# Performance work log

Measured on AMD Instinct MI355X. Metric: run time of the kernel, lower is better.

Reference implementation:

```python
import jax, jax.numpy as jnp
import numpy as np

NUM_NODES = 8192
IN_FEATURES = 1024
OUT_FEATURES = 512
NUM_EDGES = 262144  # avg degree 32


def setup_inputs() -> dict:
    key = jax.random.key(0)
    k_x, k_w, k_b, k_src, k_dst = jax.random.split(key, 5)
    x = jax.random.normal(k_x, (NUM_NODES, IN_FEATURES), dtype=jnp.float32)
    # torch nn.Linear layout: weight [out, in], bias [out]
    W = jax.random.normal(k_w, (OUT_FEATURES, IN_FEATURES), dtype=jnp.float32) * (1.0 / np.sqrt(IN_FEATURES))
    b = jax.random.normal(k_b, (OUT_FEATURES,), dtype=jnp.float32) * 0.01
    src = jax.random.randint(k_src, (NUM_EDGES,), 0, NUM_NODES, dtype=jnp.int64)
    dst = jax.random.randint(k_dst, (NUM_EDGES,), 0, NUM_NODES, dtype=jnp.int64)
    edge_index = jnp.stack([src, dst], axis=0)
    return {"x": x, "W": W, "b": b, "edge_index": edge_index, "num_nodes": NUM_NODES}


def reference(x, W, b, edge_index, num_nodes):
    # Faithful to the torch module: build dense adjacency from edge list
    # (duplicate edges collapse to 1.0 via assignment semantics),
    # linear, (dropout p=0 -> identity), dense adj @ hidden, relu.
    adj = jnp.zeros((num_nodes, num_nodes), dtype=x.dtype)
    adj = adj.at[edge_index[0], edge_index[1]].set(1.0)
    hidden = x @ W.T + b            # [N, out]
    support = adj @ hidden          # [N, out] aggregation over neighbors
    return jax.nn.relu(support)
```

## Files before the change

kernel.cpp:

```cpp
#include <hip/hip_runtime.h>

#define N_NODES 8192
#define IN_F    1024
#define OUT_F   512
#define N_EDGES 262144
#define STRIDE  96
#define NBLK    32

#define HID_OFF     0u
#define WB_OFF      8388608u
#define DEG_OFF     9437184u
#define COL_OFF     9469952u
#define BH_OFF      12615680u
#define BO_OFF      13664256u
#define MAX_DEG     STRIDE

typedef short  bf16x8 __attribute__((ext_vector_type(8)));
typedef float  f32x4  __attribute__((ext_vector_type(4)));

__device__ __forceinline__ unsigned f2bf(float f) {
    unsigned u = __float_as_uint(f);
    u += 0x7fffu + ((u >> 16) & 1u);
    return u >> 16;
}

__device__ __forceinline__ float bflo(unsigned u) { return __uint_as_float(u << 16); }
__device__ __forceinline__ float bfhi(unsigned u) { return __uint_as_float(u & 0xffff0000u); }

__device__ __forceinline__ void ld_lds16(const void* g, void* l) {
    __builtin_amdgcn_global_load_lds(
        (const __attribute__((address_space(1))) void*)g,
        (__attribute__((address_space(3))) void*)l, 16, 0, 0);
}

#define NW8 (OUT_F * IN_F / 8)
__global__ __launch_bounds__(256) void prep(const float* __restrict__ w,
                                            unsigned short* __restrict__ wb) {
    int i = blockIdx.x * blockDim.x + threadIdx.x;
    const f32x4* p = (const f32x4*)w + (size_t)i * 2;
    f32x4 v0 = __builtin_nontemporal_load(p);
    f32x4 v1 = __builtin_nontemporal_load(p + 1);
    uint4 o;
    o.x = f2bf(v0.x) | (f2bf(v0.y) << 16);
    o.y = f2bf(v0.z) | (f2bf(v0.w) << 16);
    o.z = f2bf(v1.x) | (f2bf(v1.y) << 16);
    o.w = f2bf(v1.z) | (f2bf(v1.w) << 16);
    *((uint4*)wb + i) = o;
}

__global__ __launch_bounds__(256) void hist_a(const int* __restrict__ src,
                                              int* __restrict__ blkhist) {
    __shared__ int h[N_NODES];
    const int b   = blockIdx.x;
    const int tid = threadIdx.x;
    for (int i = tid; i < N_NODES; i += 256) h[i] = 0;
    __syncthreads();
    const int e0 = b * (N_EDGES / NBLK);
#pragma unroll
    for (int j = 0; j < N_EDGES / NBLK / 256; ++j)
        atomicAdd(&h[src[e0 + j * 256 + tid]], 1);
    __syncthreads();
    for (int i = tid; i < N_NODES; i += 256)
        blkhist[b * N_NODES + i] = h[i];
}

__global__ __launch_bounds__(256) void scan_b(const int* __restrict__ blkhist,
                                              int* __restrict__ boff,
                                              int* __restrict__ deg) {
    const int i = blockIdx.x * 256 + threadIdx.x;
    int s = 0;
#pragma unroll
    for (int b = 0; b < NBLK; ++b) {
        int t = blkhist[b * N_NODES + i];
        boff[b * N_NODES + i] = s;
        s += t;
    }
    deg[i] = s;
}

__global__ __launch_bounds__(256) void place_c(const int* __restrict__ src,
                                               const int* __restrict__ dst,
                                               const int* __restrict__ boff,
                                               int* __restrict__ col) {
    __shared__ int h[N_NODES];
    const int b   = blockIdx.x;
    const int tid = threadIdx.x;
    for (int i = tid; i < N_NODES; i += 256) h[i] = 0;
    __syncthreads();
    const int e0 = b * (N_EDGES / NBLK);
#pragma unroll
    for (int j = 0; j < N_EDGES / NBLK / 256; ++j) {
        int e = e0 + j * 256 + tid;
        int s = src[e];
        int r = boff[b * N_NODES + s] + atomicAdd(&h[s], 1);
        if (r < STRIDE) col[s * STRIDE + r] = dst[e];
    }
}

__global__ __launch_bounds__(256, 6) void gemm_mfma(const float* __restrict__ X,
                                                    const unsigned short* __restrict__ Wb,
                                                    const float* __restrict__ bias,
                                                    unsigned short* __restrict__ H) {
    __shared__ unsigned short As[64 * 64];
    __shared__ unsigned short Bs[64 * 64];

    const int bid  = blockIdx.x;
    const int tid  = threadIdx.x;
    const int lane = tid & 63;
    const int wave = tid >> 6;
    const int row0 = (bid & 127) * 64;
    const int col0 = (bid >> 7) * 64;
    const int wm   = (wave & 1) * 32;
    const int wn   = (wave >> 1) * 32;
    const int fm   = lane & 15;
    const int fm7  = fm & 7;
    const int q    = lane >> 4;

    f32x4 acc[2][2];
#pragma unroll
    for (int i = 0; i < 2; ++i)
#pragma unroll
        for (int j = 0; j < 2; ++j) acc[i][j] = (f32x4)0.f;

    const int ar   = tid >> 2;
    const int ak4  = tid & 3;
    const int ar7  = ar & 7;
    unsigned short* As_w0 = As + ar * 64 + ((ak4 * 2)     ^ ar7) * 8;
    unsigned short* As_w1 = As + ar * 64 + ((ak4 * 2 + 1) ^ ar7) * 8;
    const float* xrow = &X[(size_t)(row0 + ar) * IN_F + ak4 * 16];

    const int br = tid >> 3;
    const int bk = ((tid & 7) ^ (br & 7)) * 8;

    for (int k0 = 0; k0 < IN_F; k0 += 64) {
        const f32x4* px = (const f32x4*)(xrow + k0);
        f32x4 v0 = px[0], v1 = px[1], v2 = px[2], v3 = px[3];
        ld_lds16(Wb + (size_t)(col0 + br) * IN_F + k0 + bk,      Bs + tid * 8);
        ld_lds16(Wb + (size_t)(col0 + br + 32) * IN_F + k0 + bk, Bs + (tid + 256) * 8);
        uint4 pa, pb;
        pa.x = f2bf(v0.x) | (f2bf(v0.y) << 16);
        pa.y = f2bf(v0.z) | (f2bf(v0.w) << 16);
        pa.z = f2bf(v1.x) | (f2bf(v1.y) << 16);
        pa.w = f2bf(v1.z) | (f2bf(v1.w) << 16);
        pb.x = f2bf(v2.x) | (f2bf(v2.y) << 16);
        pb.y = f2bf(v2.z) | (f2bf(v2.w) << 16);
        pb.z = f2bf(v3.x) | (f2bf(v3.y) << 16);
        pb.w = f2bf(v3.z) | (f2bf(v3.w) << 16);
        *(uint4*)As_w0 = pa;
        *(uint4*)As_w1 = pb;
        __syncthreads();

#pragma unroll
        for (int s = 0; s < 2; ++s) {
            const int kq = s * 4 + q;
            bf16x8 a[2], b[2];
#pragma unroll
            for (int mi = 0; mi < 2; ++mi)
                a[mi] = *(const bf16x8*)&As[(((wm + mi * 16 + fm) << 3) + (kq ^ fm7)) << 3];
#pragma unroll
            for (int ni = 0; ni < 2; ++ni)
                b[ni] = *(const bf16x8*)&Bs[(((wn + ni * 16 + fm) << 3) + (kq ^ fm7)) << 3];
#pragma unroll
            for (int mi = 0; mi < 2; ++mi)
#pragma unroll
                for (int ni = 0; ni < 2; ++ni)
                    acc[mi][ni] = __builtin_amdgcn_mfma_f32_16x16x32_bf16(
                        a[mi], b[ni], acc[mi][ni], 0, 0, 0);
        }
        __syncthreads();
    }

    const int cm = (lane >> 4) * 4;
#pragma unroll
    for (int ni = 0; ni < 2; ++ni) {
        const int c = col0 + wn + ni * 16 + fm;
        const float bv = bias[c];
#pragma unroll
        for (int mi = 0; mi < 2; ++mi) {
#pragma unroll
            for (int r = 0; r < 4; ++r) {
                const int row = row0 + wm + mi * 16 + cm + r;
                H[(size_t)row * OUT_F + c] = (unsigned short)f2bf(acc[mi][ni][r] + bv);
            }
        }
    }
}

__global__ __launch_bounds__(256) void aggregate(const unsigned short* __restrict__ H,
                                                 const int* __restrict__ dg,
                                                 const int* __restrict__ col,
                                                 float* __restrict__ out) {
    __shared__ int nbr[4][MAX_DEG];
    __shared__ int uniq[4][MAX_DEG];
    __shared__ int wcnt[4];
    const int wave = threadIdx.x >> 6;
    const int lane = threadIdx.x & 63;
    const int v    = blockIdx.x * 4 + wave;
    int d = dg[v];
    if (d > MAX_DEG) d = MAX_DEG;

    if (lane == 0) wcnt[wave] = 0;
    int id0 = -1, id1 = -1;
    if (lane < d)      { id0 = col[v * STRIDE + lane];      nbr[wave][lane]      = id0; }
    if (64 + lane < d) { id1 = col[v * STRIDE + 64 + lane]; nbr[wave][64 + lane] = id1; }
    __builtin_amdgcn_wave_barrier();

    bool k0 = (lane < d);
    const int lim0 = k0 ? lane : 0;
    for (int j = 0; j < lim0; ++j) k0 = k0 & (nbr[wave][j] != id0);
    bool k1 = (64 + lane < d);
    const int lim1 = k1 ? (64 + lane) : 0;
    for (int j = 0; j < lim1; ++j) k1 = k1 & (nbr[wave][j] != id1);
    if (k0) uniq[wave][atomicAdd(&wcnt[wave], 1)] = id0;
    if (k1) uniq[wave][atomicAdd(&wcnt[wave], 1)] = id1;
    __builtin_amdgcn_wave_barrier();
    const int n  = wcnt[wave];
    const int f0 = lane * 8;

    float a0=0,a1=0,a2=0,a3=0,a4=0,a5=0,a6=0,a7=0;
    int e = 0;
    for (; e + 4 <= n; e += 4) {
        const int i0 = uniq[wave][e], i1 = uniq[wave][e+1],
                  i2 = uniq[wave][e+2], i3 = uniq[wave][e+3];
        uint4 h0 = *(const uint4*)&H[(size_t)i0 * OUT_F + f0];
        uint4 h1 = *(const uint4*)&H[(size_t)i1 * OUT_F + f0];
        uint4 h2 = *(const uint4*)&H[(size_t)i2 * OUT_F + f0];
        uint4 h3 = *(const uint4*)&H[(size_t)i3 * OUT_F + f0];
        a0 += bflo(h0.x)+bflo(h1.x)+bflo(h2.x)+bflo(h3.x);
        a1 += bfhi(h0.x)+bfhi(h1.x)+bfhi(h2.x)+bfhi(h3.x);
        a2 += bflo(h0.y)+bflo(h1.y)+bflo(h2.y)+bflo(h3.y);
        a3 += bfhi(h0.y)+bfhi(h1.y)+bfhi(h2.y)+bfhi(h3.y);
        a4 += bflo(h0.z)+bflo(h1.z)+bflo(h2.z)+bflo(h3.z);
        a5 += bfhi(h0.z)+bfhi(h1.z)+bfhi(h2.z)+bfhi(h3.z);
        a6 += bflo(h0.w)+bflo(h1.w)+bflo(h2.w)+bflo(h3.w);
        a7 += bfhi(h0.w)+bfhi(h1.w)+bfhi(h2.w)+bfhi(h3.w);
    }
    for (; e < n; ++e) {
        uint4 h0 = *(const uint4*)&H[(size_t)uniq[wave][e] * OUT_F + f0];
        a0 += bflo(h0.x); a1 += bfhi(h0.x);
        a2 += bflo(h0.y); a3 += bfhi(h0.y);
        a4 += bflo(h0.z); a5 += bfhi(h0.z);
        a6 += bflo(h0.w); a7 += bfhi(h0.w);
    }
    f32x4 o0 = {fmaxf(a0,0.f), fmaxf(a1,0.f), fmaxf(a2,0.f), fmaxf(a3,0.f)};
    f32x4 o1 = {fmaxf(a4,0.f), fmaxf(a5,0.f), fmaxf(a6,0.f), fmaxf(a7,0.f)};
    __builtin_nontemporal_store(o0, (f32x4*)&out[(size_t)v * OUT_F + f0]);
    __builtin_nontemporal_store(o1, (f32x4*)&out[(size_t)v * OUT_F + f0 + 4]);
}

extern "C" void kernel_launch(void* const* d_in, const int* in_sizes, int n_in,
                              void* d_out, int out_size, void* d_ws, size_t ws_size,
                              hipStream_t stream) {
    const float* x  = (const float*)d_in[0];
    const float* W  = (const float*)d_in[1];
    const float* b  = (const float*)d_in[2];
    const int*   ei = (const int*)d_in[3];
    float* out = (float*)d_out;

    char* ws = (char*)d_ws;
    unsigned short* H       = (unsigned short*)(ws + HID_OFF);
    unsigned short* Wb      = (unsigned short*)(ws + WB_OFF);
    int*            deg     = (int*)(ws + DEG_OFF);
    int*            col     = (int*)(ws + COL_OFF);
    int*            blkhist = (int*)(ws + BH_OFF);
    int*            boff    = (int*)(ws + BO_OFF);

    const int* src = ei;
    const int* dst = ei + N_EDGES;

    prep<<<NW8 / 256, 256, 0, stream>>>(W, Wb);
    hist_a<<<NBLK, 256, 0, stream>>>(src, blkhist);
    scan_b<<<N_NODES / 256, 256, 0, stream>>>(blkhist, boff, deg);
    place_c<<<NBLK, 256, 0, stream>>>(src, dst, boff, col);
    gemm_mfma<<<1024, 256, 0, stream>>>(x, Wb, b, H);
    aggregate<<<N_NODES / 4, 256, 0, stream>>>(H, deg, col, out);
}
```

Before: 168.8 us.

## Fuse weight prep with histogram and CSR placement with GEMM launches

Merges the weight bf16 conversion and the edge histogram into one launch, and runs the CSR column placement as extra blocks inside the GEMM launch, so independent stages share a grid and two launches disappear. It also doubles the number of histogram/placement blocks to spread the edge work across more CUs. As a cost, the GEMM blocks now reserve 32KB of shared memory (sized for the placement path) and the occupancy hint drops to 4, which can reduce GEMM residency. The scan also reads twice as many per-block histograms.

```diff
diff --git a/kernel.cpp b/kernel.cpp
--- a/kernel.cpp
+++ b/kernel.cpp
@@ -5,14 +5,15 @@
 #define OUT_F   512
 #define N_EDGES 262144
 #define STRIDE  96
-#define NBLK    32
+#define NBLK    64
+#define EPB     (N_EDGES / NBLK)
 
 #define HID_OFF     0u
 #define WB_OFF      8388608u
 #define DEG_OFF     9437184u
 #define COL_OFF     9469952u
 #define BH_OFF      12615680u
-#define BO_OFF      13664256u
+#define BO_OFF      14712832u
 #define MAX_DEG     STRIDE
 
 typedef short  bf16x8 __attribute__((ext_vector_type(8)));
@@ -34,30 +35,33 @@
 }
 
 #define NW8 (OUT_F * IN_F / 8)
-__global__ __launch_bounds__(256) void prep(const float* __restrict__ w,
-                                            unsigned short* __restrict__ wb) {
-    int i = blockIdx.x * blockDim.x + threadIdx.x;
-    const f32x4* p = (const f32x4*)w + (size_t)i * 2;
-    f32x4 v0 = __builtin_nontemporal_load(p);
-    f32x4 v1 = __builtin_nontemporal_load(p + 1);
-    uint4 o;
-    o.x = f2bf(v0.x) | (f2bf(v0.y) << 16);
-    o.y = f2bf(v0.z) | (f2bf(v0.w) << 16);
-    o.z = f2bf(v1.x) | (f2bf(v1.y) << 16);
-    o.w = f2bf(v1.z) | (f2bf(v1.w) << 16);
-    *((uint4*)wb + i) = o;
-}
-
-__global__ __launch_bounds__(256) void hist_a(const int* __restrict__ src,
-                                              int* __restrict__ blkhist) {
+__global__ __launch_bounds__(256) void prep_hist(const float* __restrict__ w,
+                                                 unsigned short* __restrict__ wb,
+                                                 const int* __restrict__ src,
+                                                 int* __restrict__ blkhist) {
     __shared__ int h[N_NODES];
-    const int b   = blockIdx.x;
+    const int bid = blockIdx.x;
     const int tid = threadIdx.x;
+
+    if (bid < 256) {
+        int i = bid * 256 + tid;
+        const f32x4* p = (const f32x4*)w + (size_t)i * 2;
+        f32x4 v0 = __builtin_nontemporal_load(p);
+        f32x4 v1 = __builtin_nontemporal_load(p + 1);
+        uint4 o;
+        o.x = f2bf(v0.x) | (f2bf(v0.y) << 16);
+        o.y = f2bf(v0.z) | (f2bf(v0.w) << 16);
+        o.z = f2bf(v1.x) | (f2bf(v1.y) << 16);
+        o.w = f2bf(v1.z) | (f2bf(v1.w) << 16);
+        *((uint4*)wb + i) = o;
+        return;
+    }
+    const int b = bid - 256;
     for (int i = tid; i < N_NODES; i += 256) h[i] = 0;
     __syncthreads();
-    const int e0 = b * (N_EDGES / NBLK);
-#pragma unroll
-    for (int j = 0; j < N_EDGES / NBLK / 256; ++j)
+    const int e0 = b * EPB;
+#pragma unroll
+    for (int j = 0; j < EPB / 256; ++j)
         atomicAdd(&h[src[e0 + j * 256 + tid]], 1);
     __syncthreads();
     for (int i = tid; i < N_NODES; i += 256)
@@ -69,7 +73,7 @@
                                               int* __restrict__ deg) {
     const int i = blockIdx.x * 256 + threadIdx.x;
     int s = 0;
-#pragma unroll
+#pragma unroll 8
     for (int b = 0; b < NBLK; ++b) {
         int t = blkhist[b * N_NODES + i];
         boff[b * N_NODES + i] = s;
@@ -78,34 +82,35 @@
     deg[i] = s;
 }
 
-__global__ __launch_bounds__(256) void place_c(const int* __restrict__ src,
-                                               const int* __restrict__ dst,
-                                               const int* __restrict__ boff,
-                                               int* __restrict__ col) {
-    __shared__ int h[N_NODES];
-    const int b   = blockIdx.x;
+__global__ __launch_bounds__(256, 4) void gemm_place(const float* __restrict__ X,
+                                                     const unsigned short* __restrict__ Wb,
+                                                     const float* __restrict__ bias,
+                                                     unsigned short* __restrict__ H,
+                                                     const int* __restrict__ src,
+                                                     const int* __restrict__ dst,
+                                                     const int* __restrict__ boff,
+                                                     int* __restrict__ col) {
+    __shared__ int smem[N_NODES];
+    const int bid = blockIdx.x;
     const int tid = threadIdx.x;
-    for (int i = tid; i < N_NODES; i += 256) h[i] = 0;
-    __syncthreads();
-    const int e0 = b * (N_EDGES / NBLK);
-#pragma unroll
-    for (int j = 0; j < N_EDGES / NBLK / 256; ++j) {
-        int e = e0 + j * 256 + tid;
-        int s = src[e];
-        int r = boff[b * N_NODES + s] + atomicAdd(&h[s], 1);
-        if (r < STRIDE) col[s * STRIDE + r] = dst[e];
-    }
-}
-
-__global__ __launch_bounds__(256, 6) void gemm_mfma(const float* __restrict__ X,
-                                                    const unsigned short* __restrict__ Wb,
-                                                    const float* __restrict__ bias,
-                                                    unsigned short* __restrict__ H) {
-    __shared__ unsigned short As[64 * 64];
-    __shared__ unsigned short Bs[64 * 64];
-
-    const int bid  = blockIdx.x;
-    const int tid  = threadIdx.x;
+
+    if (bid >= 1024) {
+        const int b = bid - 1024;
+        for (int i = tid; i < N_NODES; i += 256) smem[i] = 0;
+        __syncthreads();
+        const int e0 = b * EPB;
+#pragma unroll
+        for (int j = 0; j < EPB / 256; ++j) {
+            int e = e0 + j * 256 + tid;
+            int s = src[e];
+            int r = boff[b * N_NODES + s] + atomicAdd(&smem[s], 1);
+            if (r < STRIDE) col[s * STRIDE + r] = dst[e];
+        }
+        return;
+    }
+
+    unsigned short* As = (unsigned short*)smem;
+    unsigned short* Bs = (unsigned short*)smem + 4096;
     const int lane = tid & 63;
     const int wave = tid >> 6;
     const int row0 = (bid & 127) * 64;
@@ -268,10 +273,8 @@
     const int* src = ei;
     const int* dst = ei + N_EDGES;
 
-    prep<<<NW8 / 256, 256, 0, stream>>>(W, Wb);
-    hist_a<<<NBLK, 256, 0, stream>>>(src, blkhist);
+    prep_hist<<<256 + NBLK, 256, 0, stream>>>(W, Wb, src, blkhist);
     scan_b<<<N_NODES / 256, 256, 0, stream>>>(blkhist, boff, deg);
-    place_c<<<NBLK, 256, 0, stream>>>(src, dst, boff, col);
-    gemm_mfma<<<1024, 256, 0, stream>>>(x, Wb, b, H);
+    gemm_place<<<1024 + NBLK, 256, 0, stream>>>(x, Wb, b, H, src, dst, boff, col);
     aggregate<<<N_NODES / 4, 256, 0, stream>>>(H, deg, col, out);
 }
```

Measured after the change: 153.1 us. -9.3%, faster.
